# Optimization experiments

Measured on AMD Instinct MI355X. Metric: run time of the kernel, lower is better.

Reference implementation:

```python
import jax, jax.numpy as jnp
import numpy as np

K = 3   # bil_filt_size
NL = 1  # n_layers (bil_filt_size == 2*n_layers + 1 required for shape consistency)


def _conv3d_relu(x, w, b):
    # Conv3d(1,1,kernel=3,stride=1,valid) + ReLU, NCDHW layout
    y = jax.lax.conv_general_dilated(
        x, w, window_strides=(1, 1, 1), padding='VALID',
        dimension_numbers=('NCDHW', 'OIDHW', 'NCDHW'))
    return jax.nn.relu(y + b[None, :, None, None, None])


def setup_inputs() -> dict:
    key = jax.random.key(0)
    ks = jax.random.split(key, 7)
    B, D, H, W = 2, 18, 128, 128
    Dout = D - 2 * NL            # 16
    M = B * Dout * H * W         # 524288 per-voxel neighborhoods
    s = K + 2 * NL               # 5: conv shrinks s -> K
    x = jax.random.normal(ks[0], (B, 1, D, H, W), dtype=jnp.float32)
    domain_neighbor = jax.random.uniform(ks[1], (M, 1, s, s, s), dtype=jnp.float32)
    guide_im = jax.random.normal(ks[2], (M, 1, s, s, s), dtype=jnp.float32)
    dom_w = jax.random.normal(ks[3], (1, 1, 3, 3, 3), dtype=jnp.float32) * 0.1
    dom_b = jnp.full((1,), 0.01, dtype=jnp.float32)
    rng_w = jax.random.normal(ks[4], (1, 1, 3, 3, 3), dtype=jnp.float32) * 0.1
    rng_b = jnp.full((1,), 0.01, dtype=jnp.float32)
    return {'x': x, 'domain_neighbor': domain_neighbor, 'guide_im': guide_im,
            'dom_w': dom_w, 'dom_b': dom_b, 'rng_w': rng_w, 'rng_b': rng_b}


def reference(x, domain_neighbor, guide_im, dom_w, dom_b, rng_w, rng_b):
    B, _, D, H, W = x.shape
    Dout = D - 2 * NL
    # learned bilateral weights per voxel: [M,1,K,K,K]
    domain_kernel = _conv3d_relu(domain_neighbor, dom_w, dom_b)
    range_kernel = _conv3d_relu(guide_im, rng_w, rng_b)
    weights = domain_kernel * range_kernel + 1e-10
    # unfold order in torch is (B, C=1, Dout, H, W, k, k, k) -> reshape(-1,1,k,k,k)
    Wr = weights.reshape(B, Dout, H, W, K, K, K)
    pad = K // 2
    # pad H and W only (no depth padding), matching F.pad(..., (p,p,p,p,0,0))
    xp = jnp.pad(x[:, 0], ((0, 0), (0, 0), (pad, pad), (pad, pad)))  # [B,D,H+2p,W+2p]
    # fused weighted local sum: avoid materializing the K^3-unfolded tensor
    num = jnp.zeros((B, Dout, H, W), dtype=x.dtype)
    for i in range(K):
        for j in range(K):
            for l in range(K):
                num = num + Wr[..., i, j, l] * xp[:, i:i + Dout, j:j + H, l:l + W]
    den = Wr.sum(axis=(-3, -2, -1))
    return (num / den)[:, None]  # [B,1,Dout,H,W]
```

## Files before the change

kernel.cpp:

```cpp
#include <hip/hip_runtime.h>


#define VPB 64
#define REC 125
#define CHUNK_F4 2000

__global__ __launch_bounds__(64) void jbf_kernel(
    const float* __restrict__ x,
    const float* __restrict__ dom,
    const float* __restrict__ gui,
    const float* __restrict__ dom_w,
    const float* __restrict__ dom_b,
    const float* __restrict__ rng_w,
    const float* __restrict__ rng_b,
    float* __restrict__ out)
{
    __shared__ float sm[VPB * REC];
    const int lane = threadIdx.x;
    const int m0   = blockIdx.x * VPB;
    const int m    = m0 + lane;

    float wd[27], wr[27];
#pragma unroll
    for (int i = 0; i < 27; ++i) { wd[i] = dom_w[i]; wr[i] = rng_w[i]; }
    const float bd = dom_b[0], br = rng_b[0];

    {
        const float4* src = (const float4*)(dom + (size_t)m0 * REC);
        float4* dst = (float4*)sm;
#pragma unroll
        for (int k = 0; k < 31; ++k) dst[k * 64 + lane] = src[k * 64 + lane];
        if (lane < CHUNK_F4 - 31 * 64) dst[31 * 64 + lane] = src[31 * 64 + lane];
    }
    __syncthreads();

    float dkv[27];
#pragma unroll
    for (int i = 0; i < 27; ++i) dkv[i] = 0.f;
    {
        const float* rec = sm + lane * REC;
#pragma unroll
        for (int z = 0; z < 5; ++z)
#pragma unroll
            for (int r = 0; r < 5; ++r)
#pragma unroll
                for (int c = 0; c < 5; ++c) {
                    const float v = rec[z * 25 + r * 5 + c];
#pragma unroll
                    for (int i = 0; i < 3; ++i) {
                        const int a = z - i; if (a < 0 || a > 2) continue;
#pragma unroll
                        for (int j = 0; j < 3; ++j) {
                            const int b = r - j; if (b < 0 || b > 2) continue;
#pragma unroll
                            for (int l = 0; l < 3; ++l) {
                                const int cc = c - l; if (cc < 0 || cc > 2) continue;
                                dkv[(i * 3 + j) * 3 + l] =
                                    fmaf(v, wd[(a * 3 + b) * 3 + cc],
                                         dkv[(i * 3 + j) * 3 + l]);
                            }
                        }
                    }
                }
    }
    __syncthreads();

    {
        const float4* src = (const float4*)(gui + (size_t)m0 * REC);
        float4* dst = (float4*)sm;
#pragma unroll
        for (int k = 0; k < 31; ++k) dst[k * 64 + lane] = src[k * 64 + lane];
        if (lane < CHUNK_F4 - 31 * 64) dst[31 * 64 + lane] = src[31 * 64 + lane];
    }
    __syncthreads();

    float rkv[27];
#pragma unroll
    for (int i = 0; i < 27; ++i) rkv[i] = 0.f;
    {
        const float* rec = sm + lane * REC;
#pragma unroll
        for (int z = 0; z < 5; ++z)
#pragma unroll
            for (int r = 0; r < 5; ++r)
#pragma unroll
                for (int c = 0; c < 5; ++c) {
                    const float v = rec[z * 25 + r * 5 + c];
#pragma unroll
                    for (int i = 0; i < 3; ++i) {
                        const int a = z - i; if (a < 0 || a > 2) continue;
#pragma unroll
                        for (int j = 0; j < 3; ++j) {
                            const int b = r - j; if (b < 0 || b > 2) continue;
#pragma unroll
                            for (int l = 0; l < 3; ++l) {
                                const int cc = c - l; if (cc < 0 || cc > 2) continue;
                                rkv[(i * 3 + j) * 3 + l] =
                                    fmaf(v, wr[(a * 3 + b) * 3 + cc],
                                         rkv[(i * 3 + j) * 3 + l]);
                            }
                        }
                    }
                }
    }

    const int w_  = m & 127;
    const int h_  = (m >> 7) & 127;
    const int dz  = (m >> 14) & 15;
    const int b_  = m >> 18;

    float num = 0.f, den = 0.f;
#pragma unroll
    for (int i = 0; i < 3; ++i) {
        const int zz = b_ * 18 + dz + i;
#pragma unroll
        for (int j = 0; j < 3; ++j) {
            const int hh = h_ - 1 + j;
            const bool okh = (unsigned)hh < 128u;
#pragma unroll
            for (int l = 0; l < 3; ++l) {
                const int ww = w_ - 1 + l;
                const bool ok = okh && ((unsigned)ww < 128u);
                const float xv = ok ? x[((size_t)zz * 128 + hh) * 128 + ww] : 0.f;
                const float wv = fmaxf(dkv[(i * 3 + j) * 3 + l] + bd, 0.f) *
                                 fmaxf(rkv[(i * 3 + j) * 3 + l] + br, 0.f) + 1e-10f;
                den += wv;
                num = fmaf(wv, xv, num);
            }
        }
    }
    out[m] = num / den;
}

extern "C" void kernel_launch(void* const* d_in, const int* in_sizes, int n_in,
                              void* d_out, int out_size, void* d_ws, size_t ws_size,
                              hipStream_t stream) {
    const float* x     = (const float*)d_in[0];
    const float* dom   = (const float*)d_in[1];
    const float* gui   = (const float*)d_in[2];
    const float* dom_w = (const float*)d_in[3];
    const float* dom_b = (const float*)d_in[4];
    const float* rng_w = (const float*)d_in[5];
    const float* rng_b = (const float*)d_in[6];
    float* outp = (float*)d_out;

    const int M = in_sizes[1] / REC;
    const int grid = M / VPB;
    jbf_kernel<<<grid, VPB, 0, stream>>>(x, dom, gui, dom_w, dom_b,
                                         rng_w, rng_b, outp);
}
```

Measured before the change: 511.8 us.

## Pipeline record loads via direct global-to-LDS DMA with persistent chunk loop

Each block now handles 16 consecutive 64-voxel chunks. Records are streamed with global_load_lds straight into two LDS buffers, one for domain and one for guide, and the next chunk's load is issued as soon as the current buffer has been consumed. Manual s_waitcnt vmcnt counts replace __syncthreads. The goal is to hide the heavy streaming of the 125-float records behind the convolution math and to skip the register round trip on the LDS copy. In exchange there are 16x fewer blocks, so parallelism drops, and correctness depends on hand-tuned waitcnt values that must match the number of outstanding loads, including the x gathers.

```diff
diff --git a/kernel.cpp b/kernel.cpp
--- a/kernel.cpp
+++ b/kernel.cpp
@@ -1,9 +1,52 @@
 #include <hip/hip_runtime.h>
 
 
-#define VPB 64
-#define REC 125
-#define CHUNK_F4 2000
+#define REC   125
+#define VPB   64
+#define NC    16
+#define BUF_F 8000
+
+__device__ __forceinline__ void dma_buf(const float* gsrc, float* lds, int lane) {
+#pragma unroll
+    for (int k = 0; k < 31; ++k) {
+        __builtin_amdgcn_global_load_lds(
+            (const __attribute__((address_space(1))) void*)(gsrc + k * 256 + lane * 4),
+            (__attribute__((address_space(3))) void*)(lds + k * 256),
+            16, 0, 0);
+    }
+    __builtin_amdgcn_global_load_lds(
+        (const __attribute__((address_space(1))) void*)(gsrc + 31 * 256 + lane),
+        (__attribute__((address_space(3))) void*)(lds + 31 * 256),
+        4, 0, 0);
+}
+
+__device__ __forceinline__ void conv555_333(const float* __restrict__ rec,
+                                            const float* __restrict__ wt,
+                                            float* __restrict__ acc) {
+#pragma unroll
+    for (int z = 0; z < 5; ++z)
+#pragma unroll
+        for (int r = 0; r < 5; ++r)
+#pragma unroll
+            for (int c = 0; c < 5; ++c) {
+                const float v = rec[z * 25 + r * 5 + c];
+#pragma unroll
+                for (int i = 0; i < 3; ++i) {
+                    const int a = z - i; if (a < 0 || a > 2) continue;
+#pragma unroll
+                    for (int j = 0; j < 3; ++j) {
+                        const int b = r - j; if (b < 0 || b > 2) continue;
+#pragma unroll
+                        for (int l = 0; l < 3; ++l) {
+                            const int cc = c - l; if (cc < 0 || cc > 2) continue;
+                            acc[(i * 3 + j) * 3 + l] =
+                                fmaf(v, wt[(a * 3 + b) * 3 + cc],
+                                     acc[(i * 3 + j) * 3 + l]);
+                        }
+                    }
+                }
+            }
+}
 
 __global__ __launch_bounds__(64) void jbf_kernel(
     const float* __restrict__ x,
@@ -15,121 +58,77 @@
     const float* __restrict__ rng_b,
     float* __restrict__ out)
 {
-    __shared__ float sm[VPB * REC];
+    __shared__ __align__(16) float A[BUF_F];
+    __shared__ __align__(16) float B[BUF_F];
     const int lane = threadIdx.x;
-    const int m0   = blockIdx.x * VPB;
-    const int m    = m0 + lane;
+    const int ch0  = blockIdx.x * NC;
 
     float wd[27], wr[27];
 #pragma unroll
     for (int i = 0; i < 27; ++i) { wd[i] = dom_w[i]; wr[i] = rng_w[i]; }
     const float bd = dom_b[0], br = rng_b[0];
 
-    {
-        const float4* src = (const float4*)(dom + (size_t)m0 * REC);
-        float4* dst = (float4*)sm;
+    dma_buf(dom + (size_t)ch0 * BUF_F, A, lane);
+    dma_buf(gui + (size_t)ch0 * BUF_F, B, lane);
+
+#pragma clang loop unroll(disable)
+    for (int c = 0; c < NC; ++c) {
+        const int ch = ch0 + c;
+        const int m  = ch * VPB + lane;
+
+        asm volatile("s_waitcnt vmcnt(32)" ::: "memory");
+
+        float dkv[27];
 #pragma unroll
-        for (int k = 0; k < 31; ++k) dst[k * 64 + lane] = src[k * 64 + lane];
-        if (lane < CHUNK_F4 - 31 * 64) dst[31 * 64 + lane] = src[31 * 64 + lane];
-    }
-    __syncthreads();
+        for (int i = 0; i < 27; ++i) dkv[i] = 0.f;
+        conv555_333(A + lane * REC, wd, dkv);
 
-    float dkv[27];
+        if (c + 1 < NC)
+            dma_buf(dom + (size_t)(ch + 1) * BUF_F, A, lane);
+
+        if (c + 1 < NC) { asm volatile("s_waitcnt vmcnt(32)" ::: "memory"); }
+        else            { asm volatile("s_waitcnt vmcnt(0)"  ::: "memory"); }
+
+        const int w_ = m & 127;
+        const int h_ = (m >> 7) & 127;
+        const int dz = (m >> 14) & 15;
+        const int b_ = m >> 18;
+        float xv[27];
 #pragma unroll
-    for (int i = 0; i < 27; ++i) dkv[i] = 0.f;
-    {
-        const float* rec = sm + lane * REC;
+        for (int i = 0; i < 3; ++i) {
+            const int zz = b_ * 18 + dz + i;
 #pragma unroll
-        for (int z = 0; z < 5; ++z)
+            for (int j = 0; j < 3; ++j) {
+                const int hh = h_ - 1 + j;
+                const bool okh = (unsigned)hh < 128u;
 #pragma unroll
-            for (int r = 0; r < 5; ++r)
-#pragma unroll
-                for (int c = 0; c < 5; ++c) {
-                    const float v = rec[z * 25 + r * 5 + c];
-#pragma unroll
-                    for (int i = 0; i < 3; ++i) {
-                        const int a = z - i; if (a < 0 || a > 2) continue;
-#pragma unroll
-                        for (int j = 0; j < 3; ++j) {
-                            const int b = r - j; if (b < 0 || b > 2) continue;
-#pragma unroll
-                            for (int l = 0; l < 3; ++l) {
-                                const int cc = c - l; if (cc < 0 || cc > 2) continue;
-                                dkv[(i * 3 + j) * 3 + l] =
-                                    fmaf(v, wd[(a * 3 + b) * 3 + cc],
-                                         dkv[(i * 3 + j) * 3 + l]);
-                            }
-                        }
-                    }
+                for (int l = 0; l < 3; ++l) {
+                    const int ww = w_ - 1 + l;
+                    const bool ok = okh && ((unsigned)ww < 128u);
+                    xv[(i * 3 + j) * 3 + l] =
+                        ok ? x[((size_t)zz * 128 + hh) * 128 + ww] : 0.f;
                 }
-    }
-    __syncthreads();
-
-    {
-        const float4* src = (const float4*)(gui + (size_t)m0 * REC);
-        float4* dst = (float4*)sm;
-#pragma unroll
-        for (int k = 0; k < 31; ++k) dst[k * 64 + lane] = src[k * 64 + lane];
-        if (lane < CHUNK_F4 - 31 * 64) dst[31 * 64 + lane] = src[31 * 64 + lane];
-    }
-    __syncthreads();
-
-    float rkv[27];
-#pragma unroll
-    for (int i = 0; i < 27; ++i) rkv[i] = 0.f;
-    {
-        const float* rec = sm + lane * REC;
-#pragma unroll
-        for (int z = 0; z < 5; ++z)
-#pragma unroll
-            for (int r = 0; r < 5; ++r)
-#pragma unroll
-                for (int c = 0; c < 5; ++c) {
-                    const float v = rec[z * 25 + r * 5 + c];
-#pragma unroll
-                    for (int i = 0; i < 3; ++i) {
-                        const int a = z - i; if (a < 0 || a > 2) continue;
-#pragma unroll
-                        for (int j = 0; j < 3; ++j) {
-                            const int b = r - j; if (b < 0 || b > 2) continue;
-#pragma unroll
-                            for (int l = 0; l < 3; ++l) {
-                                const int cc = c - l; if (cc < 0 || cc > 2) continue;
-                                rkv[(i * 3 + j) * 3 + l] =
-                                    fmaf(v, wr[(a * 3 + b) * 3 + cc],
-                                         rkv[(i * 3 + j) * 3 + l]);
-                            }
-                        }
-                    }
-                }
-    }
-
-    const int w_  = m & 127;
-    const int h_  = (m >> 7) & 127;
-    const int dz  = (m >> 14) & 15;
-    const int b_  = m >> 18;
-
-    float num = 0.f, den = 0.f;
-#pragma unroll
-    for (int i = 0; i < 3; ++i) {
-        const int zz = b_ * 18 + dz + i;
-#pragma unroll
-        for (int j = 0; j < 3; ++j) {
-            const int hh = h_ - 1 + j;
-            const bool okh = (unsigned)hh < 128u;
-#pragma unroll
-            for (int l = 0; l < 3; ++l) {
-                const int ww = w_ - 1 + l;
-                const bool ok = okh && ((unsigned)ww < 128u);
-                const float xv = ok ? x[((size_t)zz * 128 + hh) * 128 + ww] : 0.f;
-                const float wv = fmaxf(dkv[(i * 3 + j) * 3 + l] + bd, 0.f) *
-                                 fmaxf(rkv[(i * 3 + j) * 3 + l] + br, 0.f) + 1e-10f;
-                den += wv;
-                num = fmaf(wv, xv, num);
             }
         }
+
+        float rkv[27];
+#pragma unroll
+        for (int i = 0; i < 27; ++i) rkv[i] = 0.f;
+        conv555_333(B + lane * REC, wr, rkv);
+
+        float num = 0.f, den = 0.f;
+#pragma unroll
+        for (int k = 0; k < 27; ++k) {
+            const float wv = fmaxf(dkv[k] + bd, 0.f) *
+                             fmaxf(rkv[k] + br, 0.f) + 1e-10f;
+            den += wv;
+            num = fmaf(wv, xv[k], num);
+        }
+        out[m] = num / den;
+
+        if (c + 1 < NC)
+            dma_buf(gui + (size_t)(ch + 1) * BUF_F, B, lane);
     }
-    out[m] = num / den;
 }
 
 extern "C" void kernel_launch(void* const* d_in, const int* in_sizes, int n_in,
@@ -145,7 +144,7 @@
     float* outp = (float*)d_out;
 
     const int M = in_sizes[1] / REC;
-    const int grid = M / VPB;
+    const int grid = M / (VPB * NC);
     jbf_kernel<<<grid, VPB, 0, stream>>>(x, dom, gui, dom_w, dom_b,
                                          rng_w, rng_b, outp);
 }
```

Measured after the change: 540.8 us. +5.7%, slower.
